# Performance work log

Measured on AMD Instinct MI355X. Metric: run time of the kernel, lower is better.

Reference implementation:

```python
import math
import jax, jax.numpy as jnp
import numpy as np

RCR = 5.2
RCA = 3.5
ETA_R = 16.0
ETA_A = 8.0
ZETA = 32.0
NUM_SPECIES = 4
SHF_R = jnp.linspace(0.9, RCR, 17)[:-1]                      # [16]
SHF_A = jnp.linspace(0.9, RCA, 5)[:-1]                       # [4]
SHF_Z = (jnp.linspace(0.0, math.pi, 9) + math.pi / 16)[:-1]  # [8]


def _triu_index(num_species):
    i1, i2 = np.triu_indices(num_species)
    pair = np.arange(len(i1))
    ret = np.zeros((num_species, num_species), dtype=np.int32)
    ret[i1, i2] = pair
    ret[i2, i1] = pair
    return jnp.asarray(ret)

TRIU = _triu_index(NUM_SPECIES)  # [S,S] -> pair index in [0, S(S+1)/2)


def setup_inputs() -> dict:
    key = jax.random.key(0)
    k1, k2 = jax.random.split(key)
    species = jax.random.randint(k1, (64, 32), 0, NUM_SPECIES, dtype=jnp.int32)
    # spread atoms over a few Angstrom so neighbor lists are non-trivial
    coordinates = jax.random.normal(k2, (64, 32, 3), dtype=jnp.float32) * 2.0
    return {"species": species, "coordinates": coordinates}


def _cutoff_cosine(d, rc):
    # CutoffCosine: 0.5*cos(pi*d/rc)+0.5 inside cutoff, 0 outside
    return jnp.where(d <= rc, 0.5 * jnp.cos(math.pi * d / rc) + 0.5, 0.0)


def _aev(species, coordinates):
    N, A, _ = coordinates.shape
    S = NUM_SPECIES
    # vec[n,i,j] = coords[n,j] - coords[n,i]
    diff = coordinates[:, None, :, :] - coordinates[:, :, None, :]  # [N,A,A,3]
    d2 = jnp.sum(diff * diff, axis=-1)                              # [N,A,A]
    dist = jnp.sqrt(jnp.where(d2 > 0, d2, 1.0))
    eye = jnp.eye(A, dtype=bool)

    # ---- radial AEV: 0.25 * exp(-EtaR*(d-ShfR)^2) * fc(d), binned by species[j]
    rmask = (~eye) & (dist <= RCR)                                  # [N,A,A]
    fc_r = _cutoff_cosine(dist, RCR)
    g = 0.25 * jnp.exp(-ETA_R * (dist[..., None] - SHF_R) ** 2) * fc_r[..., None]
    g = g * rmask[..., None]                                        # [N,A,A,16]
    sp_onehot = jax.nn.one_hot(species, S, dtype=g.dtype)           # [N,A,S]
    radial = jnp.einsum('nijr,njs->nisr', g, sp_onehot).reshape(N, A, S * 16)

    # ---- angular AEV over triplets (i; j<k), both neighbors within Rca
    amask = (~eye) & (dist <= RCA)                                  # [N,A,A]
    fc_a = _cutoff_cosine(dist, RCA) * amask
    dot = jnp.einsum('nijc,nikc->nijk', diff, diff)                 # [N,A,A,A]
    denom = dist[:, :, :, None] * dist[:, :, None, :]
    cos_ang = jnp.clip(0.95 * dot / jnp.where(denom > 0, denom, 1.0), -0.95, 0.95)
    theta = jnp.arccos(cos_ang)                                     # [N,A,A,A]
    dmean = 0.5 * (dist[:, :, :, None] + dist[:, :, None, :])
    f1 = ((1.0 + jnp.cos(theta[..., None] - SHF_Z)) * 0.5) ** ZETA  # [N,A,A,A,8]
    f2 = jnp.exp(-ETA_A * (dmean[..., None] - SHF_A) ** 2)          # [N,A,A,A,4]
    jk = jnp.arange(A)
    tmask = amask[:, :, :, None] & amask[:, :, None, :] & (jk[:, None] < jk[None, :])
    fc_pair = fc_a[:, :, :, None] * fc_a[:, :, None, :] * tmask
    # sublength ordering: ShfA outer, ShfZ inner (EtaA, Zeta are scalars)
    term = 2.0 * f2[..., :, None] * f1[..., None, :]                # [N,A,A,A,4,8]
    term = (term * fc_pair[..., None, None]).reshape(N, A, A, A, 32)
    pair_idx = TRIU[species[:, :, None], species[:, None, :]]       # [N,A,A]
    pair_oh = jax.nn.one_hot(pair_idx, S * (S + 1) // 2, dtype=term.dtype)
    angular = jnp.einsum('nijku,njkp->nipu', term, pair_oh)
    angular = angular.reshape(N, A, (S * (S + 1) // 2) * 32)

    return jnp.concatenate([radial, angular], axis=-1)              # [N,A,384]


def reference(species, coordinates):
    aev = _aev(species, coordinates)
    return species, aev
```

## Files before the change

kernel.cpp:

```cpp
#include <hip/hip_runtime.h>
#include <math.h>

#define NATOMS 32
#define NMOL   64
#define MAXPC  465
#define RCRf 5.2f
#define RCAf 3.5f

__global__ __launch_bounds__(512) void aev_kernel(const int* __restrict__ species,
                                                  const float* __restrict__ coords,
                                                  float* __restrict__ out) {
    const int blk = blockIdx.x;
    const int mol = blk >> 3;
    const int i0  = (blk & 7) << 2;
    const int tid = threadIdx.x;
    const int lane = tid & 63;

    __shared__ float4   s_catom[4][NATOMS];
    __shared__ float2   s_cfs[4][NATOMS];
    __shared__ float2   s_dfr[4][NATOMS];
    __shared__ int      s_sp[NATOMS];
    __shared__ unsigned s_rec[4][MAXPC*8];
    __shared__ int      s_cnt[4][10], s_rank[4][10], s_nn[4];

    if (tid < 40)               ((int*)s_cnt)[tid]      = 0;
    else if (tid < 80)          ((int*)s_rank)[tid-40]  = 0;

    if (tid < 128) {
        const int c = tid >> 5, j = tid & 31, i = i0 + c;
        const float* cb = coords + (size_t)mol*NATOMS*3;
        float dx = cb[j*3+0] - cb[i*3+0];
        float dy = cb[j*3+1] - cb[i*3+1];
        float dz = cb[j*3+2] - cb[i*3+2];
        float d2 = dx*dx + dy*dy + dz*dz;
        float d  = sqrtf(d2 > 0.f ? d2 : 1.f);
        int  spv = species[mol*NATOMS + j];
        bool self = (j == i);
        float fr  = (!self && d <= RCRf) ? (0.5f*__cosf(((float)M_PI/RCRf)*d) + 0.5f) : 0.f;
        float fca = (!self && d <= RCAf) ? (0.5f*__cosf(((float)M_PI/RCAf)*d) + 0.5f) : 0.f;
        s_dfr[c][j] = make_float2(d, fr);
        if (tid < 32) s_sp[j] = spv;
        unsigned long long m = __ballot(fca > 0.f);
        unsigned mh = (unsigned)(m >> (lane & 32));
        int lpos = lane & 31;
        int ci = __popc(mh & ((1u << lpos) - 1u));
        if (fca > 0.f) {
            s_catom[c][ci] = make_float4(dx, dy, dz, d);
            s_cfs[c][ci]   = make_float2(fca, (float)spv);
        }
        if (lpos == 0) s_nn[c] = __popc(mh);
    }
    __syncthreads();

    const int c  = tid >> 7;
    const int l  = tid & 127;
    const int nn = s_nn[c];
    const int cnt = (nn*(nn-1)) >> 1;
    const int M   = 2*nn - 1;

    if (tid < 4) out[mol*NATOMS + i0 + tid] = (float)s_sp[i0 + tid];

    for (int p = l; p < cnt; p += 128) {
        float t = sqrtf((float)(M*M - 8*p));
        int jj = (int)(((float)M - t) * 0.5f);
        jj = max(0, min(jj, nn-2));
        while (jj*(2*nn-jj-1)/2 > p) --jj;
        while ((jj+1)*(2*nn-jj-2)/2 <= p) ++jj;
        int kk = p - jj*(2*nn-jj-1)/2 + jj + 1;
        int sj = (int)s_cfs[c][jj].y, sk = (int)s_cfs[c][kk].y;
        int lo = min(sj, sk), hi = max(sj, sk);
        int px = ((lo*(9-lo)) >> 1) + (hi - lo);
        atomicAdd(&s_cnt[c][px], 1);
    }
    __syncthreads();

    int cc[10], pf[10];
    {
        int run = 0;
        #pragma unroll
        for (int b = 0; b < 10; ++b) { cc[b] = s_cnt[c][b]; pf[b] = run; run += cc[b]; }
    }

    const float CZ[8] = { 0.98078528f,  0.83146961f,  0.55557023f,  0.19509032f,
                         -0.19509032f, -0.55557023f, -0.83146961f, -0.98078528f};
    const float SZ[8] = { 0.19509032f,  0.55557023f,  0.83146961f,  0.98078528f,
                          0.98078528f,  0.83146961f,  0.55557023f,  0.19509032f};
    const float SHA[4] = {0.9f, 1.55f, 2.2f, 2.85f};

    for (int p = l; p < cnt; p += 128) {
        float t = sqrtf((float)(M*M - 8*p));
        int jj = (int)(((float)M - t) * 0.5f);
        jj = max(0, min(jj, nn-2));
        while (jj*(2*nn-jj-1)/2 > p) --jj;
        while ((jj+1)*(2*nn-jj-2)/2 <= p) ++jj;
        int kk = p - jj*(2*nn-jj-1)/2 + jj + 1;
        float4 aj = s_catom[c][jj], ak = s_catom[c][kk];
        float2 fj = s_cfs[c][jj],  fk = s_cfs[c][kk];
        float fc2 = 2.f * fj.x * fk.x;
        float dot = aj.x*ak.x + aj.y*ak.y + aj.z*ak.z;
        float cv = 0.95f * dot * __builtin_amdgcn_rcpf(aj.w * ak.w);
        cv = fminf(0.95f, fmaxf(-0.95f, cv));
        float sv = sqrtf(1.f - cv*cv);
        float dmean = 0.5f * (aj.w + ak.w);
        int sj = (int)fj.y, sk = (int)fk.y;
        int lo = min(sj, sk), hi = max(sj, sk);
        int px = ((lo*(9-lo)) >> 1) + (hi - lo);
        float f1[8];
        #pragma unroll
        for (int z = 0; z < 8; ++z) {
            float x = 0.5f + 0.5f*(cv*CZ[z] + sv*SZ[z]);
            float q = x*x; q *= q; q *= q; q *= q; q *= q;
            f1[z] = q;
        }
        uint4 u;
        u.x = ((__float_as_uint(f1[0]) + 0x8000u) >> 16) | (((__float_as_uint(f1[1]) + 0x8000u) >> 16) << 16);
        u.y = ((__float_as_uint(f1[2]) + 0x8000u) >> 16) | (((__float_as_uint(f1[3]) + 0x8000u) >> 16) << 16);
        u.z = ((__float_as_uint(f1[4]) + 0x8000u) >> 16) | (((__float_as_uint(f1[5]) + 0x8000u) >> 16) << 16);
        u.w = ((__float_as_uint(f1[6]) + 0x8000u) >> 16) | (((__float_as_uint(f1[7]) + 0x8000u) >> 16) << 16);
        float4 v2;
        float dm0 = dmean - SHA[0], dm1 = dmean - SHA[1];
        float dm2 = dmean - SHA[2], dm3 = dmean - SHA[3];
        v2.x = __expf(-8.f*dm0*dm0) * fc2;
        v2.y = __expf(-8.f*dm1*dm1) * fc2;
        v2.z = __expf(-8.f*dm2*dm2) * fc2;
        v2.w = __expf(-8.f*dm3*dm3) * fc2;
        int slot = pf[px] + atomicAdd(&s_rank[c][px], 1);
        unsigned* r = &s_rec[c][slot*8];
        *(uint4*)r        = u;
        *(float4*)(r + 4) = v2;
    }
    __syncthreads();

    float* outbase = out + NMOL*NATOMS;

    #pragma unroll
    for (int k = 0; k < 3; ++k) {
        int g = tid + (k << 9);
        if (g < 1280) {
            int ec = g / 320;
            int f  = g - ec*320;
            int b = f >> 5, a = (f >> 3) & 3, z = f & 7;
            int base = 0, bc;
            #pragma unroll
            for (int q = 0; q < 10; ++q) { int v = s_cnt[ec][q]; base += (q < b) ? v : 0; }
            bc = s_cnt[ec][b];
            const unsigned* rb = &s_rec[ec][0];
            const int zh = z >> 1, hi16 = (z & 1);
            float acc = 0.f;
            #pragma unroll 4
            for (int q = base; q < base + bc; ++q) {
                unsigned uf = rb[q*8 + zh];
                float f1 = __uint_as_float(hi16 ? (uf & 0xFFFF0000u) : (uf << 16));
                float f2 = __uint_as_float(rb[q*8 + 4 + a]);
                acc += f1 * f2;
            }
            outbase[(size_t)(mol*NATOMS + i0 + ec)*384 + 64 + f] = acc;
        }
    }

    if (tid >= 256) {
        int t = tid - 256;
        int rc = t >> 6, f = t & 63;
        int rs = f >> 4;
        float shr = 0.9f + 0.26875f * (float)(f & 15);
        float racc = 0.f;
        #pragma unroll 8
        for (int j = 0; j < NATOMS; ++j) {
            float2 dfr = s_dfr[rc][j];
            float dm = dfr.x - shr;
            racc += (s_sp[j] == rs) ? 0.25f * __expf(-16.f*dm*dm) * dfr.y : 0.f;
        }
        outbase[(size_t)(mol*NATOMS + i0 + rc)*384 + f] = racc;
    }
}

extern "C" void kernel_launch(void* const* d_in, const int* in_sizes, int n_in,
                              void* d_out, int out_size, void* d_ws, size_t ws_size,
                              hipStream_t stream) {
    const int*   species = (const int*)d_in[0];
    const float* coords  = (const float*)d_in[1];
    float*       out     = (float*)d_out;
    aev_kernel<<<NMOL*8, 512, 0, stream>>>(species, coords, out);
}
```

Baseline: 16.40 us.

## Assign one center atom per 256-thread block and overlap radial with pair counting

Restructures the kernel from 512-thread blocks covering four center atoms each to 256-thread blocks covering a single center atom, giving 2048 blocks and less shared memory per block. The radial AEV is now computed by a separate wavefront during the species-pair counting phase rather than after the angular reduction. Prefix sums come from scalar registers instead of a per-bin array. The aim is better occupancy and load balance across atoms with different neighbor counts, at the cost of redoing per-molecule setup work in each block and leaving some threads idle in the final reduction.

```diff
diff --git a/kernel.cpp b/kernel.cpp
--- a/kernel.cpp
+++ b/kernel.cpp
@@ -7,79 +7,92 @@
 #define RCRf 5.2f
 #define RCAf 3.5f
 
-__global__ __launch_bounds__(512) void aev_kernel(const int* __restrict__ species,
-                                                  const float* __restrict__ coords,
-                                                  float* __restrict__ out) {
-    const int blk = blockIdx.x;
-    const int mol = blk >> 3;
-    const int i0  = (blk & 7) << 2;
+__global__ __launch_bounds__(256, 8) void aev_kernel(const int* __restrict__ species,
+                                                     const float* __restrict__ coords,
+                                                     float* __restrict__ out) {
+    const int bid = blockIdx.x;
+    const int n = bid >> 5;
+    const int i = bid & 31;
     const int tid = threadIdx.x;
-    const int lane = tid & 63;
 
-    __shared__ float4   s_catom[4][NATOMS];
-    __shared__ float2   s_cfs[4][NATOMS];
-    __shared__ float2   s_dfr[4][NATOMS];
+    __shared__ float4   s_catom[NATOMS];
+    __shared__ float2   s_cfs[NATOMS];
+    __shared__ float2   s_dfr[NATOMS];
     __shared__ int      s_sp[NATOMS];
-    __shared__ unsigned s_rec[4][MAXPC*8];
-    __shared__ int      s_cnt[4][10], s_rank[4][10], s_nn[4];
+    __shared__ unsigned s_rec[MAXPC*8];
+    __shared__ int      s_cnt[10], s_rank[10], s_nn;
 
-    if (tid < 40)               ((int*)s_cnt)[tid]      = 0;
-    else if (tid < 80)          ((int*)s_rank)[tid-40]  = 0;
+    if (tid >= 64 && tid < 74)  s_cnt[tid-64]  = 0;
+    if (tid >= 74 && tid < 84)  s_rank[tid-74] = 0;
 
-    if (tid < 128) {
-        const int c = tid >> 5, j = tid & 31, i = i0 + c;
-        const float* cb = coords + (size_t)mol*NATOMS*3;
-        float dx = cb[j*3+0] - cb[i*3+0];
-        float dy = cb[j*3+1] - cb[i*3+1];
-        float dz = cb[j*3+2] - cb[i*3+2];
-        float d2 = dx*dx + dy*dy + dz*dz;
-        float d  = sqrtf(d2 > 0.f ? d2 : 1.f);
-        int  spv = species[mol*NATOMS + j];
-        bool self = (j == i);
-        float fr  = (!self && d <= RCRf) ? (0.5f*__cosf(((float)M_PI/RCRf)*d) + 0.5f) : 0.f;
-        float fca = (!self && d <= RCAf) ? (0.5f*__cosf(((float)M_PI/RCAf)*d) + 0.5f) : 0.f;
-        s_dfr[c][j] = make_float2(d, fr);
-        if (tid < 32) s_sp[j] = spv;
-        unsigned long long m = __ballot(fca > 0.f);
-        unsigned mh = (unsigned)(m >> (lane & 32));
-        int lpos = lane & 31;
-        int ci = __popc(mh & ((1u << lpos) - 1u));
-        if (fca > 0.f) {
-            s_catom[c][ci] = make_float4(dx, dy, dz, d);
-            s_cfs[c][ci]   = make_float2(fca, (float)spv);
+    if (tid < 64) {
+        float fca_v = 0.f, sv = 0.f;
+        float4 av = make_float4(0.f, 0.f, 0.f, 0.f);
+        if (tid < NATOMS) {
+            const float* cb = coords + (size_t)n*NATOMS*3;
+            float dx = cb[tid*3+0] - cb[i*3+0];
+            float dy = cb[tid*3+1] - cb[i*3+1];
+            float dz = cb[tid*3+2] - cb[i*3+2];
+            float d2 = dx*dx + dy*dy + dz*dz;
+            float d  = sqrtf(d2 > 0.f ? d2 : 1.f);
+            bool self = (tid == i);
+            float fr = (!self && d <= RCRf) ? (0.5f*__cosf(((float)M_PI/RCRf)*d) + 0.5f) : 0.f;
+            fca_v    = (!self && d <= RCAf) ? (0.5f*__cosf(((float)M_PI/RCAf)*d) + 0.5f) : 0.f;
+            int spv = species[n*NATOMS + tid];
+            s_dfr[tid] = make_float2(d, fr);
+            s_sp[tid]  = spv;
+            av = make_float4(dx, dy, dz, d);
+            sv = (float)spv;
         }
-        if (lpos == 0) s_nn[c] = __popc(mh);
+        unsigned long long m = __ballot(fca_v > 0.f);
+        int ci = (int)__popcll(m & ((1ull << tid) - 1ull));
+        if (fca_v > 0.f) { s_catom[ci] = av; s_cfs[ci] = make_float2(fca_v, sv); }
+        if (tid == 0) s_nn = (int)__popcll(m);
     }
     __syncthreads();
 
-    const int c  = tid >> 7;
-    const int l  = tid & 127;
-    const int nn = s_nn[c];
+    const int nn  = s_nn;
     const int cnt = (nn*(nn-1)) >> 1;
     const int M   = 2*nn - 1;
+    float* oa = out + NMOL*NATOMS + (size_t)bid * 384;
 
-    if (tid < 4) out[mol*NATOMS + i0 + tid] = (float)s_sp[i0 + tid];
+    if (tid == 255) out[bid] = (float)s_sp[i];
 
-    for (int p = l; p < cnt; p += 128) {
+    for (int p = tid; p < cnt; p += 256) {
         float t = sqrtf((float)(M*M - 8*p));
         int jj = (int)(((float)M - t) * 0.5f);
         jj = max(0, min(jj, nn-2));
         while (jj*(2*nn-jj-1)/2 > p) --jj;
         while ((jj+1)*(2*nn-jj-2)/2 <= p) ++jj;
         int kk = p - jj*(2*nn-jj-1)/2 + jj + 1;
-        int sj = (int)s_cfs[c][jj].y, sk = (int)s_cfs[c][kk].y;
+        int sj = (int)s_cfs[jj].y, sk = (int)s_cfs[kk].y;
         int lo = min(sj, sk), hi = max(sj, sk);
         int px = ((lo*(9-lo)) >> 1) + (hi - lo);
-        atomicAdd(&s_cnt[c][px], 1);
+        atomicAdd(&s_cnt[px], 1);
+    }
+
+    if (tid >= 128 && tid < 192) {
+        const int f  = tid - 128;
+        const int rs = f >> 4;
+        const float shr = 0.9f + 0.26875f * (float)(f & 15);
+        float racc = 0.f;
+        #pragma unroll 8
+        for (int j = 0; j < NATOMS; ++j) {
+            float2 dfr = s_dfr[j];
+            float dm = dfr.x - shr;
+            racc += (s_sp[j] == rs) ? 0.25f * __expf(-16.f*dm*dm) * dfr.y : 0.f;
+        }
+        oa[f] = racc;
     }
     __syncthreads();
 
-    int cc[10], pf[10];
-    {
-        int run = 0;
-        #pragma unroll
-        for (int b = 0; b < 10; ++b) { cc[b] = s_cnt[c][b]; pf[b] = run; run += cc[b]; }
-    }
+    const int c0 = s_cnt[0], c1 = s_cnt[1], c2 = s_cnt[2], c3 = s_cnt[3], c4 = s_cnt[4];
+    const int c5 = s_cnt[5], c6 = s_cnt[6], c7 = s_cnt[7], c8 = s_cnt[8], c9 = s_cnt[9];
+    #define PREFIX(B) ( ((B) > 0 ? c0 : 0) + ((B) > 1 ? c1 : 0) + ((B) > 2 ? c2 : 0) \
+                      + ((B) > 3 ? c3 : 0) + ((B) > 4 ? c4 : 0) + ((B) > 5 ? c5 : 0) \
+                      + ((B) > 6 ? c6 : 0) + ((B) > 7 ? c7 : 0) + ((B) > 8 ? c8 : 0) )
+    #define COUNT(B)  ( (B)==0?c0 : (B)==1?c1 : (B)==2?c2 : (B)==3?c3 : (B)==4?c4 \
+                      : (B)==5?c5 : (B)==6?c6 : (B)==7?c7 : (B)==8?c8 : c9 )
 
     const float CZ[8] = { 0.98078528f,  0.83146961f,  0.55557023f,  0.19509032f,
                          -0.19509032f, -0.55557023f, -0.83146961f, -0.98078528f};
@@ -87,15 +100,15 @@
                           0.98078528f,  0.83146961f,  0.55557023f,  0.19509032f};
     const float SHA[4] = {0.9f, 1.55f, 2.2f, 2.85f};
 
-    for (int p = l; p < cnt; p += 128) {
+    for (int p = tid; p < cnt; p += 256) {
         float t = sqrtf((float)(M*M - 8*p));
         int jj = (int)(((float)M - t) * 0.5f);
         jj = max(0, min(jj, nn-2));
         while (jj*(2*nn-jj-1)/2 > p) --jj;
         while ((jj+1)*(2*nn-jj-2)/2 <= p) ++jj;
         int kk = p - jj*(2*nn-jj-1)/2 + jj + 1;
-        float4 aj = s_catom[c][jj], ak = s_catom[c][kk];
-        float2 fj = s_cfs[c][jj],  fk = s_cfs[c][kk];
+        float4 aj = s_catom[jj], ak = s_catom[kk];
+        float2 fj = s_cfs[jj],  fk = s_cfs[kk];
         float fc2 = 2.f * fj.x * fk.x;
         float dot = aj.x*ak.x + aj.y*ak.y + aj.z*ak.z;
         float cv = 0.95f * dot * __builtin_amdgcn_rcpf(aj.w * ak.w);
@@ -124,54 +137,45 @@
         v2.y = __expf(-8.f*dm1*dm1) * fc2;
         v2.z = __expf(-8.f*dm2*dm2) * fc2;
         v2.w = __expf(-8.f*dm3*dm3) * fc2;
-        int slot = pf[px] + atomicAdd(&s_rank[c][px], 1);
-        unsigned* r = &s_rec[c][slot*8];
+        int slot = PREFIX(px) + atomicAdd(&s_rank[px], 1);
+        unsigned* r = &s_rec[slot*8];
         *(uint4*)r        = u;
         *(float4*)(r + 4) = v2;
     }
     __syncthreads();
 
-    float* outbase = out + NMOL*NATOMS;
-
-    #pragma unroll
-    for (int k = 0; k < 3; ++k) {
-        int g = tid + (k << 9);
-        if (g < 1280) {
-            int ec = g / 320;
-            int f  = g - ec*320;
-            int b = f >> 5, a = (f >> 3) & 3, z = f & 7;
-            int base = 0, bc;
-            #pragma unroll
-            for (int q = 0; q < 10; ++q) { int v = s_cnt[ec][q]; base += (q < b) ? v : 0; }
-            bc = s_cnt[ec][b];
-            const unsigned* rb = &s_rec[ec][0];
-            const int zh = z >> 1, hi16 = (z & 1);
-            float acc = 0.f;
-            #pragma unroll 4
-            for (int q = base; q < base + bc; ++q) {
-                unsigned uf = rb[q*8 + zh];
-                float f1 = __uint_as_float(hi16 ? (uf & 0xFFFF0000u) : (uf << 16));
-                float f2 = __uint_as_float(rb[q*8 + 4 + a]);
-                acc += f1 * f2;
-            }
-            outbase[(size_t)(mol*NATOMS + i0 + ec)*384 + 64 + f] = acc;
+    {
+        const int g = tid;
+        const int b = g >> 5, a = (g >> 3) & 3, z = g & 7;
+        const int base = PREFIX(b), bc = COUNT(b);
+        const int zh = z >> 1, hi16 = (z & 1);
+        float acc = 0.f;
+        #pragma unroll 4
+        for (int q = base; q < base + bc; ++q) {
+            unsigned uf = s_rec[q*8 + zh];
+            float f1 = __uint_as_float(hi16 ? (uf & 0xFFFF0000u) : (uf << 16));
+            float f2 = __uint_as_float(s_rec[q*8 + 4 + a]);
+            acc += f1 * f2;
         }
+        oa[64 + g] = acc;
     }
-
-    if (tid >= 256) {
-        int t = tid - 256;
-        int rc = t >> 6, f = t & 63;
-        int rs = f >> 4;
-        float shr = 0.9f + 0.26875f * (float)(f & 15);
-        float racc = 0.f;
-        #pragma unroll 8
-        for (int j = 0; j < NATOMS; ++j) {
-            float2 dfr = s_dfr[rc][j];
-            float dm = dfr.x - shr;
-            racc += (s_sp[j] == rs) ? 0.25f * __expf(-16.f*dm*dm) * dfr.y : 0.f;
+    if (tid >= 192) {
+        const int g = tid + 64;
+        const int b = g >> 5, a = (g >> 3) & 3, z = g & 7;
+        const int base = PREFIX(b), bc = COUNT(b);
+        const int zh = z >> 1, hi16 = (z & 1);
+        float acc = 0.f;
+        #pragma unroll 4
+        for (int q = base; q < base + bc; ++q) {
+            unsigned uf = s_rec[q*8 + zh];
+            float f1 = __uint_as_float(hi16 ? (uf & 0xFFFF0000u) : (uf << 16));
+            float f2 = __uint_as_float(s_rec[q*8 + 4 + a]);
+            acc += f1 * f2;
         }
-        outbase[(size_t)(mol*NATOMS + i0 + rc)*384 + f] = racc;
+        oa[64 + g] = acc;
     }
+    #undef PREFIX
+    #undef COUNT
 }
 
 extern "C" void kernel_launch(void* const* d_in, const int* in_sizes, int n_in,
@@ -180,5 +184,5 @@
     const int*   species = (const int*)d_in[0];
     const float* coords  = (const float*)d_in[1];
     float*       out     = (float*)d_out;
-    aev_kernel<<<NMOL*8, 512, 0, stream>>>(species, coords, out);
+    aev_kernel<<<NMOL * NATOMS, 256, 0, stream>>>(species, coords, out);
 }
```

Measured after the change: 17.09 us. +4.2%, slower.
